# Kernel optimization log

Measured on AMD Instinct MI355X. Metric: run time of the kernel, lower is better.

Reference implementation:

```python
import jax, jax.numpy as jnp
import numpy as np

NL = 6        # num_layers
V = 512       # pad_vocab_size (d_model)
H = 8         # nhead
HD = V // H   # head dim
DFF = 2048    # dim_feedforward
MAXLEN = 1024 # max distance for relative-position embedding
B = 8
L = 1024
EPS = 1e-5


def _ln(x, g, b):
    m = jnp.mean(x, axis=-1, keepdims=True)
    v = jnp.mean(jnp.square(x - m), axis=-1, keepdims=True)
    return (x - m) * jax.lax.rsqrt(v + EPS) * g + b


def setup_inputs() -> dict:
    key = jax.random.key(0)
    ks = jax.random.split(key, 16)
    s = 0.02
    rn = lambda k, shp: (jax.random.normal(k, shp) * s).astype(jnp.float32)
    return {
        "x": jax.random.uniform(ks[0], (B, L, V), jnp.float32),
        "dist_emb": rn(ks[1], (MAXLEN + 1, H)),
        "in_proj_w": rn(ks[2], (NL, 3 * V, V)),
        "in_proj_b": rn(ks[3], (NL, 3 * V)),
        "out_w": rn(ks[4], (NL, V, V)),
        "out_b": rn(ks[5], (NL, V)),
        "lin1_w": rn(ks[6], (NL, DFF, V)),
        "lin1_b": rn(ks[7], (NL, DFF)),
        "lin2_w": rn(ks[8], (NL, V, DFF)),
        "lin2_b": rn(ks[9], (NL, V)),
        "ln1_g": jnp.ones((NL, V), jnp.float32),
        "ln1_b": jnp.zeros((NL, V), jnp.float32),
        "ln2_g": jnp.ones((NL, V), jnp.float32),
        "ln2_b": jnp.zeros((NL, V), jnp.float32),
        "lnf_g": jnp.ones((V,), jnp.float32),
        "lnf_b": jnp.zeros((V,), jnp.float32),
    }


def _forward(x, dist_emb, in_proj_w, in_proj_b, out_w, out_b,
             lin1_w, lin1_b, lin2_w, lin2_b,
             ln1_g, ln1_b, ln2_g, ln2_b, lnf_g, lnf_b):
    bsz, seqlen, _ = x.shape
    idx = jnp.arange(seqlen)
    dist = jnp.clip(jnp.abs(idx[None, :] - idx[:, None]), 0, MAXLEN)  # (L, L)
    bias = jnp.transpose(dist_emb[dist], (2, 0, 1))[None]  # (1, H, L, L)
    causal = idx[None, :] <= idx[:, None]                   # allow j <= i
    bias = jnp.where(causal[None, None], bias, -jnp.inf)
    kpm = ~jnp.any(x != 0, axis=2)                          # (B, L) key padding
    bias = jnp.where(kpm[:, None, None, :], -jnp.inf, bias)  # (B, H, L, L)

    out = x  # eval mode: dropouts are identity
    scale = 1.0 / np.sqrt(HD)
    for l in range(NL):
        # --- self attention (post-norm TransformerEncoderLayer) ---
        qkv = out @ in_proj_w[l].T + in_proj_b[l]            # (B, L, 3V)
        q, k, v = jnp.split(qkv, 3, axis=-1)
        q = q.reshape(bsz, seqlen, H, HD)
        k = k.reshape(bsz, seqlen, H, HD)
        v = v.reshape(bsz, seqlen, H, HD)
        scores = jnp.einsum('bqhd,bkhd->bhqk', q, k) * scale + bias
        probs = jax.nn.softmax(scores, axis=-1)
        attn = jnp.einsum('bhqk,bkhd->bqhd', probs, v).reshape(bsz, seqlen, V)
        attn = attn @ out_w[l].T + out_b[l]
        out = _ln(out + attn, ln1_g[l], ln1_b[l])
        # --- feed forward (gelu) ---
        h = jax.nn.gelu(out @ lin1_w[l].T + lin1_b[l], approximate=False)
        ff = h @ lin2_w[l].T + lin2_b[l]
        out = _ln(out + ff, ln2_g[l], ln2_b[l])
    return _ln(out, lnf_g, lnf_b)


def reference(x, dist_emb, in_proj_w, in_proj_b, out_w, out_b,
              lin1_w, lin1_b, lin2_w, lin2_b,
              ln1_g, ln1_b, ln2_g, ln2_b, lnf_g, lnf_b):
    return _forward(x, dist_emb, in_proj_w, in_proj_b, out_w, out_b,
                    lin1_w, lin1_b, lin2_w, lin2_b,
                    ln1_g, ln1_b, ln2_g, ln2_b, lnf_g, lnf_b)
```

## Files before the change

kernel.cpp:

```cpp
#include <hip/hip_runtime.h>
#include <hip/hip_bf16.h>
#include <math.h>

#define NL 6
#define V 512
#define H 8
#define HD 64
#define DFF 2048
#define MAXLEN 1024
#define B 8
#define L 1024
#define M (B*L)
#define EPS 1e-5f
#define LOG2E 1.44269504088896f

typedef __hip_bfloat16 bf16;
typedef __attribute__((ext_vector_type(8))) short s8v;
typedef __attribute__((ext_vector_type(4))) float f4v;

__device__ __forceinline__ float b2f(bf16 v){ return __bfloat162float(v); }
__device__ __forceinline__ bf16 f2b(float v){ return __float2bfloat16(v); }
__device__ __forceinline__ unsigned short f2bu(float v){
  return __builtin_bit_cast(unsigned short, __float2bfloat16(v));
}
__device__ __forceinline__ float usf(unsigned short u){
  union{unsigned int i; float f;} c; c.i = ((unsigned int)u)<<16; return c.f;
}

__device__ __forceinline__ float ldin(const void* p, size_t i, int bf){
  if(bf) return b2f(((const bf16*)p)[i]);
  return ((const float*)p)[i];
}

__device__ __forceinline__ void ldin8f(const void* p, size_t e, int bf, float* o){
  if(bf){
    union{uint4 v; unsigned short u[8];} c;
    c.v = *(const uint4*)((const bf16*)p + e);
    #pragma unroll
    for(int i=0;i<8;i++) o[i]=usf(c.u[i]);
  }else{
    const float* f=(const float*)p+e;
    float4 a=*(const float4*)f, b=*(const float4*)(f+4);
    o[0]=a.x;o[1]=a.y;o[2]=a.z;o[3]=a.w;o[4]=b.x;o[5]=b.y;o[6]=b.z;o[7]=b.w;
  }
}

__device__ __forceinline__ uint4 ldw8(const void* W, size_t e, int bf){
  if(bf) return *(const uint4*)((const bf16*)W + e);
  const float* p = (const float*)W + e;
  float4 f0 = *(const float4*)p;
  float4 f1 = *(const float4*)(p+4);
  union { unsigned short u[8]; uint4 v; } r;
  r.u[0]=f2bu(f0.x); r.u[1]=f2bu(f0.y); r.u[2]=f2bu(f0.z); r.u[3]=f2bu(f0.w);
  r.u[4]=f2bu(f1.x); r.u[5]=f2bu(f1.y); r.u[6]=f2bu(f1.z); r.u[7]=f2bu(f1.w);
  return r.v;
}

__device__ __forceinline__ void async16(const bf16* g, unsigned short* l){
  __builtin_amdgcn_global_load_lds((const __attribute__((address_space(1))) void*)g,
                                   (__attribute__((address_space(3))) void*)l, 16, 0, 0);
}

__global__ void k_detect(const void* ones, int* flag){
  unsigned int u = *(const unsigned int*)ones;
  flag[0] = (u == 0x3F803F80u) ? 1 : 0;
  flag[1] = 1;
}

__global__ __launch_bounds__(256) void k_conv(const void* __restrict__ src,
                                              bf16* __restrict__ dst,
                                              const int* __restrict__ flag, int n){
  int bf = *flag;
  int e = (blockIdx.x*256 + threadIdx.x)*8;
  if(e >= n) return;
  if(bf){
    *(uint4*)(dst+e) = *(const uint4*)((const bf16*)src + e);
  }else{
    const float* s = (const float*)src + e;
    float4 a = *(const float4*)s, b2 = *(const float4*)(s+4);
    union{uint4 v; unsigned short u[8];} c;
    c.u[0]=f2bu(a.x); c.u[1]=f2bu(a.y); c.u[2]=f2bu(a.z); c.u[3]=f2bu(a.w);
    c.u[4]=f2bu(b2.x);c.u[5]=f2bu(b2.y);c.u[6]=f2bu(b2.z);c.u[7]=f2bu(b2.w);
    *(uint4*)(dst+e) = c.v;
  }
}

__global__ __launch_bounds__(256) void k_cast_kpm(const void* __restrict__ x,
                                                 const int* __restrict__ flag,
                                                 bf16* __restrict__ cur,
                                                 float* __restrict__ kpm){
  int bf = *flag;
  int row = blockIdx.x; int t = threadIdx.x;
  __shared__ int nz;
  if(t==0) nz = 0;
  __syncthreads();
  int fl = 0;
  for(int e=t; e<V; e+=256){
    float f = ldin(x, (size_t)row*V+e, bf);
    cur[(size_t)row*V+e] = f2b(f);
    if(f != 0.f) fl = 1;
  }
  if(fl) atomicOr(&nz, 1);
  __syncthreads();
  if(t==0) kpm[row] = nz ? 0.f : 1.f;
}

template<int BN, int WM, int WN, int TM, int TN>
__global__ __launch_bounds__(256) void k_gemm(const bf16* __restrict__ A,
                                              const void* __restrict__ W,
                                              const void* __restrict__ bias,
                                              const int* __restrict__ flag,
                                              bf16* __restrict__ C,
                                              int Ndim, int K, int gelu,
                                              size_t w_off, size_t b_off){
  constexpr int TILE = (128+BN)*64;
  constexpr int ES  = BN + 8;
  __shared__ unsigned short lds[2*TILE];
  int bf = *flag;
  int t = threadIdx.x;
  int rb = blockIdx.x*128, cb = blockIdx.y*BN;
  int lane = t & 63, w = t >> 6;
  int wm = w % WM, wn = w / WM;
  int quad = lane >> 4, fid = lane & 15;

  f4v acc[TM][TN];
  #pragma unroll
  for(int i=0;i<TM;i++)
    #pragma unroll
    for(int j=0;j<TN;j++){ f4v z = {0.f,0.f,0.f,0.f}; acc[i][j] = z; }

  auto stage = [&](int kt, int bsel){
    unsigned short* Ad = lds + bsel*TILE;
    unsigned short* Bd = Ad + 128*64;
    int k0 = kt*64;
    #pragma unroll
    for(int i=0;i<4;i++){
      int r = w*32 + i*8 + (lane>>3);
      const bf16* g = A + (size_t)(rb+r)*K + k0 + (((lane&7)^(r&7))<<3);
      async16(g, Ad + (w*32 + i*8)*64);
    }
    if(bf){
      #pragma unroll
      for(int i=0;i<BN/32;i++){
        int r = w*(BN/4) + i*8 + (lane>>3);
        const bf16* g = (const bf16*)W + w_off + (size_t)(cb+r)*K + k0 + (((lane&7)^(r&7))<<3);
        async16(g, Bd + (w*(BN/4) + i*8)*64);
      }
    }else{
      const int tpr = 256/BN;
      int sr = t/tpr;
      int sc0 = (t%tpr)*(64/tpr);
      #pragma unroll
      for(int c=0;c<64/tpr;c+=8){
        uint4 d = ldw8(W, w_off + (size_t)(cb+sr)*K + k0 + sc0 + c, 0);
        int chunk = (sc0+c)>>3;
        *(uint4*)&Bd[sr*64 + ((chunk^(sr&7))<<3)] = d;
      }
    }
  };

  int KT = K/64;
  stage(0, 0);
  __syncthreads();
  int cur = 0;
  for(int kt=0;kt<KT;kt++){
    if(kt+1<KT) stage(kt+1, cur^1);
    unsigned short* As = lds + cur*TILE;
    unsigned short* Bs = As + 128*64;
    #pragma unroll
    for(int h=0;h<2;h++){
      s8v av[TM], bv[TN];
      #pragma unroll
      for(int tm=0;tm<TM;tm++){
        int r = wm*(TM*16) + tm*16 + fid;
        av[tm] = *(const s8v*)&As[r*64 + (((h*4+quad)^(r&7))<<3)];
      }
      #pragma unroll
      for(int tn=0;tn<TN;tn++){
        int c = wn*(TN*16) + tn*16 + fid;
        bv[tn] = *(const s8v*)&Bs[c*64 + (((h*4+quad)^(c&7))<<3)];
      }
      #pragma unroll
      for(int tm=0;tm<TM;tm++)
        #pragma unroll
        for(int tn=0;tn<TN;tn++)
          acc[tm][tn] = __builtin_amdgcn_mfma_f32_16x16x32_bf16(av[tm], bv[tn], acc[tm][tn], 0,0,0);
    }
    __syncthreads();
    cur ^= 1;
  }

  float bvv[TN];
  #pragma unroll
  for(int tn=0;tn<TN;tn++)
    bvv[tn] = ldin(bias, b_off + cb + wn*(TN*16) + tn*16 + fid, bf);
  unsigned short* E = lds;
  #pragma unroll
  for(int tn=0;tn<TN;tn++){
    int col = wn*(TN*16) + tn*16 + fid;
    #pragma unroll
    for(int tm=0;tm<TM;tm++)
      #pragma unroll
      for(int rg=0; rg<4; rg++){
        int row = wm*(TM*16) + tm*16 + quad*4 + rg;
        float v = acc[tm][tn][rg] + bvv[tn];
        if(gelu) v = 0.5f*v*(1.f+erff(v*0.70710678118f));
        E[row*ES + col] = f2bu(v);
      }
  }
  __syncthreads();
  int row = t>>1, c0 = (t&1)*(BN/2);
  bf16* cp = C + (size_t)(rb+row)*Ndim + cb + c0;
  #pragma unroll
  for(int c=0;c<BN/2;c+=8)
    *(uint4*)(cp + c) = *(const uint4*)&E[row*ES + c0 + c];
}

__global__ __launch_bounds__(512) void k_attn(const bf16* __restrict__ qkv,
                                              const void* __restrict__ dist_emb,
                                              const int* __restrict__ flag,
                                              const float* __restrict__ kpm,
                                              bf16* __restrict__ out){
  int bf = *flag;
  int t = threadIdx.x;
  int p = blockIdx.x;
  int bh = blockIdx.y; int b = bh>>3, h = bh&7;
  int wg = t>>8, tg = t&255;
  int w = tg>>6, lane = tg&63, quad = lane>>4, fid = lane&15;
  int ww = t>>6;

  __shared__ unsigned short Ks[2][64][70];
  __shared__ unsigned short Vt[2][64][70];
  __shared__ unsigned short PsRaw[8*16*70];
  __shared__ float distc[L];
  __shared__ float kflagS[2][64];
  __shared__ float mlX[4][16][2];

  int qt0 = p, qt1 = 15-p;
  int c0 = qt0+1, c1 = qt1+1;
  int I0 = (c0+1)>>1, IT = I0 + ((c1+1)>>1);

  int dmax = c1*64;
  for(int i=t;i<dmax;i+=512) distc[i] = ldin(dist_emb,(size_t)i*H+h,bf) * LOG2E;

  int r  = tg>>2, dc = (tg&3)*16;
  int d0 = (tg&15)*4, jj = (tg>>4)*4;
  uint4 kr0, kr1; uint2 vb[4]; float kf;

  auto tileJ = [&](int i)->int{
    if(i < 0 || i >= IT) return -1;
    if(i < I0){ int jt = 2*i + wg; return (jt < c0) ? jt : -1; }
    int jt = 2*(i-I0) + wg; return (jt < c1) ? jt : -1;
  };

  auto loadrg = [&](int j0){
    size_t kbase = (size_t)(b*L+j0+r)*(3*V) + h*HD + dc;
    kr0 = *(const uint4*)(qkv + kbase + V);
    kr1 = *(const uint4*)(qkv + kbase + V + 8);
    #pragma unroll
    for(int k2=0;k2<4;k2++)
      vb[k2] = *(const uint2*)(qkv + (size_t)(b*L+j0+jj+k2)*(3*V) + 2*V + h*HD + d0);
    kf = (tg < 64) ? kpm[b*L + j0 + tg] : 0.f;
  };

  auto store_tile = [&](){
    *(uint4*)&Ks[wg][r][dc]   = kr0;
    *(uint4*)&Ks[wg][r][dc+8] = kr1;
    const unsigned short* v0 = (const unsigned short*)&vb[0];
    const unsigned short* v1 = (const unsigned short*)&vb[1];
    const unsigned short* v2 = (const unsigned short*)&vb[2];
    const unsigned short* v3 = (const unsigned short*)&vb[3];
    #pragma unroll
    for(int i2=0;i2<4;i2++){
      unsigned short o[4] = {v0[i2], v1[i2], v2[i2], v3[i2]};
      *(uint2*)&Vt[wg][d0+i2][jj] = *(uint2*)o;
    }
    if(tg < 64) kflagS[wg][tg] = kf;
  };

  s8v aq0, aq1;
  auto loadQ = [&](int rbase){
    int qrow = rbase + w*16 + fid;
    const bf16* qp = qkv + (size_t)(b*L+qrow)*(3*V) + h*HD;
    aq0 = *(const s8v*)(qp + quad*8);
    aq1 = *(const s8v*)(qp + 32 + quad*8);
  };

  float mrow[4], lrow[4];
  f4v Oc[4];
  #pragma unroll
  for(int q2=0;q2<4;q2++){ mrow[q2]=-1e30f; lrow[q2]=0.f;
                           f4v z={0.f,0.f,0.f,0.f}; Oc[q2]=z; }

  float* Om = (float*)PsRaw;
  auto mergeOut = [&](int rbase){
    if(wg==1){
      #pragma unroll
      for(int nt=0;nt<4;nt++)
        #pragma unroll
        for(int rg=0;rg<4;rg++)
          Om[(w*16 + quad*4+rg)*68 + nt*16+fid] = Oc[nt][rg];
      if(fid==0){
        #pragma unroll
        for(int rg=0;rg<4;rg++){
          mlX[w][quad*4+rg][0] = mrow[rg];
          mlX[w][quad*4+rg][1] = lrow[rg];
        }
      }
    }
    __syncthreads();
    if(wg==0){
      #pragma unroll
      for(int rg=0;rg<4;rg++){
        float mB = mlX[w][quad*4+rg][0], lB = mlX[w][quad*4+rg][1];
        float mM = fmaxf(mrow[rg], mB);
        float msub = (mM <= -1e29f) ? 0.f : mM;
        float sA = __builtin_amdgcn_exp2f(mrow[rg] - msub);
        float sB = __builtin_amdgcn_exp2f(mB - msub);
        float lm = lrow[rg]*sA + lB*sB;
        float inv = (lm > 0.f) ? 1.f/lm : 0.f;
        int row = rbase + w*16 + quad*4 + rg;
        #pragma unroll
        for(int nt=0;nt<4;nt++){
          float ov = Oc[nt][rg]*sA + Om[(w*16 + quad*4+rg)*68 + nt*16+fid]*sB;
          out[(size_t)(b*L+row)*V + h*HD + nt*16 + fid] = f2b(ov*inv);
        }
      }
    }
  };

  int rb = qt0*64;
  loadQ(rb);

  { int j = tileJ(0); if(j>=0){ loadrg(j*64); store_tile(); }
    j = tileJ(1); if(j>=0) loadrg(j*64); }
  __syncthreads();

  for(int it=0; it<IT; it++){
    int ph = (it >= I0);
    int qt = ph ? qt1 : qt0;
    int jt = tileJ(it);
    if(jt >= 0){
      int j0 = jt*64;
      f4v Sc[4];
      #pragma unroll
      for(int nt=0;nt<4;nt++){ f4v z={0.f,0.f,0.f,0.f}; Sc[nt]=z; }
      __builtin_amdgcn_s_setprio(1);
      #pragma unroll
      for(int nt=0;nt<4;nt++){
        s8v bk0 = *(const s8v*)&Ks[wg][nt*16+fid][quad*8];
        s8v bk1 = *(const s8v*)&Ks[wg][nt*16+fid][32+quad*8];
        Sc[nt] = __builtin_amdgcn_mfma_f32_16x16x32_bf16(aq0, bk0, Sc[nt], 0,0,0);
        Sc[nt] = __builtin_amdgcn_mfma_f32_16x16x32_bf16(aq1, bk1, Sc[nt], 0,0,0);
      }
      __builtin_amdgcn_s_setprio(0);

      int diag = (jt == qt);
      float sv[4][4];
      #pragma unroll
      for(int nt=0;nt<4;nt++){
        int col_j = j0 + nt*16 + fid;
        int kmask = (kflagS[wg][nt*16+fid] != 0.f);
        #pragma unroll
        for(int rg=0;rg<4;rg++){
          int row_q = rb + w*16 + quad*4 + rg;
          int masked = kmask | (diag & (col_j > row_q));
          float bias = masked ? 0.f : distc[row_q - col_j];
          sv[nt][rg] = masked ? -1e30f : fmaf(Sc[nt][rg], 0.125f*LOG2E, bias);
        }
      }

      float alpha[4]; float nm[4]; int grow = 0;
      #pragma unroll
      for(int rg=0;rg<4;rg++){
        float tmax = fmaxf(fmaxf(sv[0][rg],sv[1][rg]),fmaxf(sv[2][rg],sv[3][rg]));
        #pragma unroll
        for(int m2=1;m2<16;m2<<=1) tmax = fmaxf(tmax, __shfl_xor(tmax, m2));
        nm[rg] = fmaxf(mrow[rg], tmax);
        grow |= (nm[rg] > mrow[rg]);
      }
      int growany = __any(grow);
      #pragma unroll
      for(int rg=0;rg<4;rg++){
        float mn = nm[rg];
        float msub = (mn <= -1e29f) ? 0.f : mn;
        alpha[rg] = growany ? __builtin_amdgcn_exp2f(mrow[rg] - msub) : 1.f;
        mrow[rg] = mn;
        float ps = 0.f;
        #pragma unroll
        for(int nt=0;nt<4;nt++){
          float pv = __builtin_amdgcn_exp2f(sv[nt][rg]-msub);
          sv[nt][rg] = pv;
          ps += pv;
        }
        #pragma unroll
        for(int m2=1;m2<16;m2<<=1) ps += __shfl_xor(ps, m2);
        lrow[rg] = lrow[rg]*alpha[rg] + ps;
      }
      if(growany){
        #pragma unroll
        for(int nt=0;nt<4;nt++)
          #pragma unroll
          for(int rg=0;rg<4;rg++)
            Oc[nt][rg] *= alpha[rg];
      }

      unsigned short* Ps = PsRaw + ww*16*70;
      #pragma unroll
      for(int nt=0;nt<4;nt++)
        #pragma unroll
        for(int rg=0;rg<4;rg++)
          Ps[(quad*4+rg)*70 + nt*16+fid] = f2bu(sv[nt][rg]);
      s8v ap0 = *(const s8v*)&Ps[fid*70 + quad*8];
      s8v ap1 = *(const s8v*)&Ps[fid*70 + 32 + quad*8];
      __builtin_amdgcn_s_setprio(1);
      #pragma unroll
      for(int nt=0;nt<4;nt++){
        s8v bv0 = *(const s8v*)&Vt[wg][nt*16+fid][quad*8];
        s8v bv1 = *(const s8v*)&Vt[wg][nt*16+fid][32+quad*8];
        Oc[nt] = __builtin_amdgcn_mfma_f32_16x16x32_bf16(ap0, bv0, Oc[nt], 0,0,0);
        Oc[nt] = __builtin_amdgcn_mfma_f32_16x16x32_bf16(ap1, bv1, Oc[nt], 0,0,0);
      }
      __builtin_amdgcn_s_setprio(0);
    }
    __syncthreads();

    if(it == I0-1){
      mergeOut(rb);
      rb = qt1*64;
      loadQ(rb);
      #pragma unroll
      for(int q2=0;q2<4;q2++){ mrow[q2]=-1e30f; lrow[q2]=0.f;
                               f4v z={0.f,0.f,0.f,0.f}; Oc[q2]=z; }
    }

    { int jn = tileJ(it+1); if(jn>=0) store_tile();
      int j2 = tileJ(it+2); if(j2>=0) loadrg(j2*64); }
    __syncthreads();
  }
  mergeOut(rb);
}

__global__ __launch_bounds__(256) void k_ln(const bf16* __restrict__ a,
                                            const bf16* __restrict__ r,
                                            const void* __restrict__ g,
                                            const void* __restrict__ be,
                                            const int* __restrict__ flag,
                                            void* __restrict__ outp,
                                            int use_r, int final_out,
                                            size_t gb_off){
  int bf = *flag;
  int t = threadIdx.x, w = t>>6, lane = t&63;
  int row = blockIdx.x*4 + w;
  size_t o = (size_t)row*V + lane*8;
  union{uint4 v; unsigned short u[8];} ua;
  ua.v = *(const uint4*)(a + o);
  float v[8];
  #pragma unroll
  for(int i=0;i<8;i++) v[i] = usf(ua.u[i]);
  if(use_r){
    union{uint4 v; unsigned short u[8];} ur;
    ur.v = *(const uint4*)(r + o);
    #pragma unroll
    for(int i=0;i<8;i++) v[i] += usf(ur.u[i]);
  }
  float s=0.f, q=0.f;
  #pragma unroll
  for(int i=0;i<8;i++){ s += v[i]; q += v[i]*v[i]; }
  #pragma unroll
  for(int m=1;m<64;m<<=1){ s += __shfl_xor(s, m); q += __shfl_xor(q, m); }
  float mean = s * (1.f/V);
  float var  = q * (1.f/V) - mean*mean;
  float rstd = 1.f / sqrtf(var + EPS);
  float gv[8], bv[8], ov[8];
  ldin8f(g,  gb_off + lane*8, bf, gv);
  ldin8f(be, gb_off + lane*8, bf, bv);
  #pragma unroll
  for(int i=0;i<8;i++) ov[i] = (v[i]-mean)*rstd*gv[i] + bv[i];
  if(final_out && !bf){
    float* op = (float*)outp + o;
    *(float4*)op     = make_float4(ov[0],ov[1],ov[2],ov[3]);
    *(float4*)(op+4) = make_float4(ov[4],ov[5],ov[6],ov[7]);
  }else{
    union{uint4 v; unsigned short u[8];} c;
    #pragma unroll
    for(int i=0;i<8;i++) c.u[i] = f2bu(ov[i]);
    *(uint4*)((bf16*)outp + o) = c.v;
  }
}

extern "C" void kernel_launch(void* const* d_in, const int* in_sizes, int n_in,
                              void* d_out, int out_size, void* d_ws, size_t ws_size,
                              hipStream_t stream){
  const void* x         = d_in[0];
  const void* dist_emb  = d_in[1];
  const void* in_proj_w = d_in[2];
  const void* in_proj_b = d_in[3];
  const void* out_w     = d_in[4];
  const void* out_b     = d_in[5];
  const void* lin1_w    = d_in[6];
  const void* lin1_b    = d_in[7];
  const void* lin2_w    = d_in[8];
  const void* lin2_b    = d_in[9];
  const void* ln1_g     = d_in[10];
  const void* ln1_bb    = d_in[11];
  const void* ln2_g     = d_in[12];
  const void* ln2_bb    = d_in[13];
  const void* lnf_g     = d_in[14];
  const void* lnf_bb    = d_in[15];

  int*   flag    = (int*)d_ws;
  int*   flagOne = flag + 1;
  float* kpm  = (float*)((char*)d_ws + 256);
  bf16*  cur  = (bf16*)(kpm + M);
  bf16*  big  = cur + (size_t)M*V;
  bf16*  attn = big + (size_t)M*(3*V);
  bf16*  proj = big + (size_t)M*DFF;
  char*  base_end = (char*)(proj + (size_t)M*V);

  const size_t S_ipw = (size_t)NL*3*V*V, S_ow = (size_t)NL*V*V;
  const size_t S_l1w = (size_t)NL*DFF*V, S_l2w = (size_t)NL*V*DFF;
  const size_t S_ipb = (size_t)NL*3*V, S_ob = (size_t)NL*V;
  const size_t S_l1b = (size_t)NL*DFF, S_l2b = (size_t)NL*V;
  const size_t SW = S_ipw + S_ow + S_l1w + S_l2w;
  const size_t SB = S_ipb + S_ob + S_l1b + S_l2b;
  size_t need = (size_t)(base_end - (char*)d_ws) + (SW + SB)*sizeof(bf16);
  int conv = (ws_size >= need);

  bf16* w_ip = (bf16*)base_end;
  bf16* w_o  = w_ip + S_ipw;
  bf16* w_l1 = w_o  + S_ow;
  bf16* w_l2 = w_l1 + S_l1w;
  bf16* b_ip = w_l2 + S_l2w;
  bf16* b_o  = b_ip + S_ipb;
  bf16* b_l1 = b_o  + S_ob;
  bf16* b_l2 = b_l1 + S_l1b;

  k_detect<<<1, 1, 0, stream>>>(lnf_g, flag);
  k_cast_kpm<<<M, 256, 0, stream>>>(x, flag, cur, kpm);

  const int* gflag = conv ? flagOne : flag;
  const void* g_ipw = conv ? (const void*)w_ip : in_proj_w;
  const void* g_ow  = conv ? (const void*)w_o  : out_w;
  const void* g_l1w = conv ? (const void*)w_l1 : lin1_w;
  const void* g_l2w = conv ? (const void*)w_l2 : lin2_w;
  const void* g_ipb = conv ? (const void*)b_ip : in_proj_b;
  const void* g_ob  = conv ? (const void*)b_o  : out_b;
  const void* g_l1b = conv ? (const void*)b_l1 : lin1_b;
  const void* g_l2b = conv ? (const void*)b_l2 : lin2_b;

  if(conv){
    auto cv = [&](const void* s, bf16* d, size_t n){
      k_conv<<<(unsigned)((n/8 + 255)/256), 256, 0, stream>>>(s, d, flag, (int)n);
    };
    cv(in_proj_w, w_ip, S_ipw);  cv(out_w, w_o, S_ow);
    cv(lin1_w, w_l1, S_l1w);     cv(lin2_w, w_l2, S_l2w);
    cv(in_proj_b, b_ip, S_ipb);  cv(out_b, b_o, S_ob);
    cv(lin1_b, b_l1, S_l1b);     cv(lin2_b, b_l2, S_l2b);
  }

  for(int l=0;l<NL;l++){
    k_gemm<128,2,2,4,4><<<dim3(M/128, (3*V)/128), 256, 0, stream>>>(
        cur, g_ipw, g_ipb, gflag, big, 3*V, V, 0,
        (size_t)l*3*V*V, (size_t)l*3*V);
    k_attn<<<dim3(8, B*H), 512, 0, stream>>>(big, dist_emb, flag, kpm, attn);
    k_gemm<64,4,1,2,4><<<dim3(M/128, V/64), 256, 0, stream>>>(
        attn, g_ow, g_ob, gflag, proj, V, V, 0,
        (size_t)l*V*V, (size_t)l*V);
    k_ln<<<M/4, 256, 0, stream>>>(cur, proj, ln1_g, ln1_bb, flag, cur, 1, 0, (size_t)l*V);
    k_gemm<128,2,2,4,4><<<dim3(M/128, DFF/128), 256, 0, stream>>>(
        cur, g_l1w, g_l1b, gflag, big, DFF, V, 1,
        (size_t)l*DFF*V, (size_t)l*DFF);
    k_gemm<64,4,1,2,4><<<dim3(M/128, V/64), 256, 0, stream>>>(
        big, g_l2w, g_l2b, gflag, proj, V, DFF, 0,
        (size_t)l*V*DFF, (size_t)l*V);
    k_ln<<<M/4, 256, 0, stream>>>(cur, proj, ln2_g, ln2_bb, flag, cur, 1, 0, (size_t)l*V);
  }
  k_ln<<<M/4, 256, 0, stream>>>(cur, cur, lnf_g, lnf_bb, flag, d_out, 0, 1, 0);
}
```

Before: 1.252 ms.

## Transpose attention score MFMA, use tanh-approx GELU, reorder attention grid

The attention kernel swaps the MFMA operands so each lane holds a single query row. The softmax max and sum then need only two cross-lane shuffles and one running max/sum per lane instead of per-register reductions over 16 lanes. The P tile store layout is changed to match. The FFN GELU switches from erf to the tanh approximation using exp2 and rcp, which cuts epilogue cost but changes numerics slightly. The attention grid is also reordered so consecutive blocks cover different batch-heads at the same query-pair index.

```diff
diff --git a/kernel.cpp b/kernel.cpp
--- a/kernel.cpp
+++ b/kernel.cpp
@@ -204,7 +204,11 @@
       for(int rg=0; rg<4; rg++){
         int row = wm*(TM*16) + tm*16 + quad*4 + rg;
         float v = acc[tm][tn][rg] + bvv[tn];
-        if(gelu) v = 0.5f*v*(1.f+erff(v*0.70710678118f));
+        if(gelu){
+          float u = v*(0.7978845608f + 0.0356774081f*v*v);
+          float e = __builtin_amdgcn_exp2f(u*(2.f*LOG2E));
+          v = v - v*__builtin_amdgcn_rcpf(e + 1.f);
+        }
         E[row*ES + col] = f2bu(v);
       }
   }
@@ -223,8 +227,8 @@
                                               bf16* __restrict__ out){
   int bf = *flag;
   int t = threadIdx.x;
-  int p = blockIdx.x;
-  int bh = blockIdx.y; int b = bh>>3, h = bh&7;
+  int bh = blockIdx.x; int b = bh>>3, h = bh&7;
+  int p = blockIdx.y;
   int wg = t>>8, tg = t&255;
   int w = tg>>6, lane = tg&63, quad = lane>>4, fid = lane&15;
   int ww = t>>6;
@@ -286,11 +290,10 @@
     aq1 = *(const s8v*)(qp + 32 + quad*8);
   };
 
-  float mrow[4], lrow[4];
+  float mrow = -1e30f, lrow = 0.f;
   f4v Oc[4];
   #pragma unroll
-  for(int q2=0;q2<4;q2++){ mrow[q2]=-1e30f; lrow[q2]=0.f;
-                           f4v z={0.f,0.f,0.f,0.f}; Oc[q2]=z; }
+  for(int q2=0;q2<4;q2++){ f4v z={0.f,0.f,0.f,0.f}; Oc[q2]=z; }
 
   float* Om = (float*)PsRaw;
   auto mergeOut = [&](int rbase){
@@ -300,29 +303,26 @@
         #pragma unroll
         for(int rg=0;rg<4;rg++)
           Om[(w*16 + quad*4+rg)*68 + nt*16+fid] = Oc[nt][rg];
-      if(fid==0){
-        #pragma unroll
-        for(int rg=0;rg<4;rg++){
-          mlX[w][quad*4+rg][0] = mrow[rg];
-          mlX[w][quad*4+rg][1] = lrow[rg];
-        }
-      }
+      if(quad==0){ mlX[w][fid][0] = mrow; mlX[w][fid][1] = lrow; }
     }
     __syncthreads();
     if(wg==0){
       #pragma unroll
       for(int rg=0;rg<4;rg++){
-        float mB = mlX[w][quad*4+rg][0], lB = mlX[w][quad*4+rg][1];
-        float mM = fmaxf(mrow[rg], mB);
+        int qr = quad*4 + rg;
+        float mB = mlX[w][qr][0], lB = mlX[w][qr][1];
+        float mA = __shfl(mrow, (lane&48)|qr);
+        float lA = __shfl(lrow, (lane&48)|qr);
+        float mM = fmaxf(mA, mB);
         float msub = (mM <= -1e29f) ? 0.f : mM;
-        float sA = __builtin_amdgcn_exp2f(mrow[rg] - msub);
+        float sA = __builtin_amdgcn_exp2f(mA - msub);
         float sB = __builtin_amdgcn_exp2f(mB - msub);
-        float lm = lrow[rg]*sA + lB*sB;
+        float lm = lA*sA + lB*sB;
         float inv = (lm > 0.f) ? 1.f/lm : 0.f;
-        int row = rbase + w*16 + quad*4 + rg;
+        int row = rbase + w*16 + qr;
         #pragma unroll
         for(int nt=0;nt<4;nt++){
-          float ov = Oc[nt][rg]*sA + Om[(w*16 + quad*4+rg)*68 + nt*16+fid]*sB;
+          float ov = Oc[nt][rg]*sA + Om[(w*16 + qr)*68 + nt*16+fid]*sB;
           out[(size_t)(b*L+row)*V + h*HD + nt*16 + fid] = f2b(ov*inv);
         }
       }
@@ -350,59 +350,58 @@
       for(int nt=0;nt<4;nt++){
         s8v bk0 = *(const s8v*)&Ks[wg][nt*16+fid][quad*8];
         s8v bk1 = *(const s8v*)&Ks[wg][nt*16+fid][32+quad*8];
-        Sc[nt] = __builtin_amdgcn_mfma_f32_16x16x32_bf16(aq0, bk0, Sc[nt], 0,0,0);
-        Sc[nt] = __builtin_amdgcn_mfma_f32_16x16x32_bf16(aq1, bk1, Sc[nt], 0,0,0);
+        Sc[nt] = __builtin_amdgcn_mfma_f32_16x16x32_bf16(bk0, aq0, Sc[nt], 0,0,0);
+        Sc[nt] = __builtin_amdgcn_mfma_f32_16x16x32_bf16(bk1, aq1, Sc[nt], 0,0,0);
       }
       __builtin_amdgcn_s_setprio(0);
 
       int diag = (jt == qt);
+      int row_q = rb + w*16 + fid;
       float sv[4][4];
       #pragma unroll
       for(int nt=0;nt<4;nt++){
-        int col_j = j0 + nt*16 + fid;
-        int kmask = (kflagS[wg][nt*16+fid] != 0.f);
         #pragma unroll
         for(int rg=0;rg<4;rg++){
-          int row_q = rb + w*16 + quad*4 + rg;
+          int kk = nt*16 + quad*4 + rg;
+          int col_j = j0 + kk;
+          int kmask = (kflagS[wg][kk] != 0.f);
           int masked = kmask | (diag & (col_j > row_q));
           float bias = masked ? 0.f : distc[row_q - col_j];
           sv[nt][rg] = masked ? -1e30f : fmaf(Sc[nt][rg], 0.125f*LOG2E, bias);
         }
       }
 
-      float alpha[4]; float nm[4]; int grow = 0;
-      #pragma unroll
-      for(int rg=0;rg<4;rg++){
-        float tmax = fmaxf(fmaxf(sv[0][rg],sv[1][rg]),fmaxf(sv[2][rg],sv[3][rg]));
-        #pragma unroll
-        for(int m2=1;m2<16;m2<<=1) tmax = fmaxf(tmax, __shfl_xor(tmax, m2));
-        nm[rg] = fmaxf(mrow[rg], tmax);
-        grow |= (nm[rg] > mrow[rg]);
-      }
-      int growany = __any(grow);
-      #pragma unroll
-      for(int rg=0;rg<4;rg++){
-        float mn = nm[rg];
-        float msub = (mn <= -1e29f) ? 0.f : mn;
-        alpha[rg] = growany ? __builtin_amdgcn_exp2f(mrow[rg] - msub) : 1.f;
-        mrow[rg] = mn;
-        float ps = 0.f;
-        #pragma unroll
-        for(int nt=0;nt<4;nt++){
+      float t0 = fmaxf(fmaxf(sv[0][0],sv[0][1]),fmaxf(sv[0][2],sv[0][3]));
+      float t1 = fmaxf(fmaxf(sv[1][0],sv[1][1]),fmaxf(sv[1][2],sv[1][3]));
+      float t2 = fmaxf(fmaxf(sv[2][0],sv[2][1]),fmaxf(sv[2][2],sv[2][3]));
+      float t3 = fmaxf(fmaxf(sv[3][0],sv[3][1]),fmaxf(sv[3][2],sv[3][3]));
+      float tmax = fmaxf(fmaxf(t0,t1),fmaxf(t2,t3));
+      tmax = fmaxf(tmax, __shfl_xor(tmax, 16));
+      tmax = fmaxf(tmax, __shfl_xor(tmax, 32));
+      float nm1 = fmaxf(mrow, tmax);
+      int growany = __any(nm1 > mrow);
+      float msub = (nm1 <= -1e29f) ? 0.f : nm1;
+      float alpha = growany ? __builtin_amdgcn_exp2f(mrow - msub) : 1.f;
+      mrow = nm1;
+      float ps = 0.f;
+      #pragma unroll
+      for(int nt=0;nt<4;nt++)
+        #pragma unroll
+        for(int rg=0;rg<4;rg++){
           float pv = __builtin_amdgcn_exp2f(sv[nt][rg]-msub);
           sv[nt][rg] = pv;
           ps += pv;
         }
-        #pragma unroll
-        for(int m2=1;m2<16;m2<<=1) ps += __shfl_xor(ps, m2);
-        lrow[rg] = lrow[rg]*alpha[rg] + ps;
-      }
+      ps += __shfl_xor(ps, 16);
+      ps += __shfl_xor(ps, 32);
+      lrow = lrow*alpha + ps;
       if(growany){
         #pragma unroll
-        for(int nt=0;nt<4;nt++)
+        for(int rg=0;rg<4;rg++){
+          float ar = __shfl(alpha, (lane&48)|(quad*4+rg));
           #pragma unroll
-          for(int rg=0;rg<4;rg++)
-            Oc[nt][rg] *= alpha[rg];
+          for(int nt=0;nt<4;nt++) Oc[nt][rg] *= ar;
+        }
       }
 
       unsigned short* Ps = PsRaw + ww*16*70;
@@ -410,7 +409,7 @@
       for(int nt=0;nt<4;nt++)
         #pragma unroll
         for(int rg=0;rg<4;rg++)
-          Ps[(quad*4+rg)*70 + nt*16+fid] = f2bu(sv[nt][rg]);
+          Ps[fid*70 + nt*16 + quad*4 + rg] = f2bu(sv[nt][rg]);
       s8v ap0 = *(const s8v*)&Ps[fid*70 + quad*8];
       s8v ap1 = *(const s8v*)&Ps[fid*70 + 32 + quad*8];
       __builtin_amdgcn_s_setprio(1);
@@ -429,9 +428,9 @@
       mergeOut(rb);
       rb = qt1*64;
       loadQ(rb);
-      #pragma unroll
-      for(int q2=0;q2<4;q2++){ mrow[q2]=-1e30f; lrow[q2]=0.f;
-                               f4v z={0.f,0.f,0.f,0.f}; Oc[q2]=z; }
+      mrow = -1e30f; lrow = 0.f;
+      #pragma unroll
+      for(int q2=0;q2<4;q2++){ f4v z={0.f,0.f,0.f,0.f}; Oc[q2]=z; }
     }
 
     { int jn = tileJ(it+1); if(jn>=0) store_tile();
@@ -563,7 +562,7 @@
     k_gemm<128,2,2,4,4><<<dim3(M/128, (3*V)/128), 256, 0, stream>>>(
         cur, g_ipw, g_ipb, gflag, big, 3*V, V, 0,
         (size_t)l*3*V*V, (size_t)l*3*V);
-    k_attn<<<dim3(8, B*H), 512, 0, stream>>>(big, dist_emb, flag, kpm, attn);
+    k_attn<<<dim3(B*H, 8), 512, 0, stream>>>(big, dist_emb, flag, kpm, attn);
     k_gemm<64,4,1,2,4><<<dim3(M/128, V/64), 256, 0, stream>>>(
         attn, g_ow, g_ob, gflag, proj, V, V, 0,
         (size_t)l*V*V, (size_t)l*V);
```

New measurement: 1.216 ms. 2.9% less time.
